# Optimization experiments

Measured on AMD Instinct MI355X. Metric: run time of the kernel, lower is better.

The kernel has to match this reference:

```python
import jax, jax.numpy as jnp
import numpy as np

B, W, K = 8, 128, 2048          # batch, window_size, n_features(=n_nodes)
D = 2 * W                        # embed_dim after the *2 in __init__ (embed_dim=None -> window_size)

def setup_inputs() -> dict:
    key = jax.random.key(0)
    k1, k2, k3, k4 = jax.random.split(key, 4)
    x = jax.random.normal(k1, (B, W, K), dtype=jnp.float32)
    # nn.Linear(2W -> D), stored as [in, out] so y = cat @ W_lin + b_lin
    lim = 1.0 / np.sqrt(2 * W)
    W_lin = jax.random.uniform(k2, (2 * W, D), dtype=jnp.float32, minval=-lim, maxval=lim)
    b_lin = jax.random.uniform(k3, (D,), dtype=jnp.float32, minval=-lim, maxval=lim)
    # a: xavier_uniform with gain=1.414 on shape (D, 1)
    a_lim = 1.414 * np.sqrt(6.0 / (D + 1))
    a = jax.random.uniform(k4, (D, 1), dtype=jnp.float32, minval=-a_lim, maxval=a_lim)
    bias = jnp.zeros((K, K), dtype=jnp.float32)
    return {"x": x, "W_lin": W_lin, "b_lin": b_lin, "a": a, "bias": bias}

def reference(x, W_lin, b_lin, a, bias):
    # x: [B, W, K] -> v: [B, K, W]
    v = jnp.transpose(x, (0, 2, 1))
    av = a[:, 0]                                  # [D]
    # lin(cat(v_i, v_j)) @ a == (v_i @ W1) @ a + (v_j @ W2) @ a + b_lin @ a
    # This avoids the O(K^2 * 2W) pairwise tensor; math identical to the original.
    W1, W2 = W_lin[:W], W_lin[W:]                 # each [W, D]
    u1 = jnp.einsum('bkw,wd,d->bk', v, W1, av)    # [B, K] source-side score
    u2 = jnp.einsum('bkw,wd,d->bk', v, W2, av)    # [B, K] target-side score
    e = u1[:, :, None] + u2[:, None, :] + jnp.dot(b_lin, av) + bias  # [B, K, K]
    attention = jax.nn.softmax(e, axis=2)         # dropout p=0.0 (eval) -> identity
    h = jax.nn.sigmoid(jnp.matmul(attention, v))  # [B, K, W]
    return jnp.transpose(h, (0, 2, 1))            # [B, W, K]
```

## Files before the change

kernel.cpp:

```cpp
#include <hip/hip_runtime.h>
#include <hip/hip_bf16.h>

#define B_ 8
#define W_ 128
#define K_ 2048
#define D_ 256
#define WX 144
#define NC 256

typedef __attribute__((ext_vector_type(8))) short bf16x8;
typedef __attribute__((ext_vector_type(4))) float f32x4;
typedef unsigned int u32;

static __device__ __forceinline__ short f2bf(float f) {
    unsigned int u = __float_as_uint(f);
    unsigned int r = (u + 0x7FFFu + ((u >> 16) & 1u)) >> 16;
    return (short)r;
}

__global__ void k_w2v(const float* __restrict__ W_lin, const float* __restrict__ a,
                      float* __restrict__ w2v) {
    int w = blockIdx.x, l = threadIdx.x;
    float4 rv = ((const float4*)(W_lin + (size_t)(W_ + w) * D_))[l];
    float4 av = ((const float4*)a)[l];
    float acc = rv.x * av.x + rv.y * av.y + rv.z * av.z + rv.w * av.w;
    for (int m = 1; m < 64; m <<= 1) acc += __shfl_xor(acc, m);
    if (l == 0) w2v[w] = acc;
}

__global__ __launch_bounds__(512) void k_pe(const float* __restrict__ x,
        const float* __restrict__ w2v, const float* __restrict__ bias,
        short* __restrict__ xbt, short* __restrict__ e2t) {
    __shared__ float sc[696];
    int tid = threadIdx.x;
    int wid = tid >> 6;
    int lane = tid & 63;

    if (blockIdx.x < 512) {
        if (tid < W_) sc[tid] = w2v[tid];
        __syncthreads();
        int q = tid & 31, cw = tid >> 5;
        int bk0 = blockIdx.x * 32;
        int b = bk0 >> 11;
        int k = (bk0 & (K_ - 1)) + q;
        const float* xp = x + ((size_t)b * W_ + cw * 8) * K_ + k;
        float xv[8];
        float acc = 0.f;
#pragma unroll
        for (int w = 0; w < 8; ++w) {
            xv[w] = xp[(size_t)w * K_];
            acc += xv[w] * sc[cw * 8 + w];
        }
        sc[128 + cw * 33 + q] = acc;
        __syncthreads();
        if (tid < 32) {
            float s = 0.f;
#pragma unroll
            for (int cc = 0; cc < 16; ++cc) s += sc[128 + cc * 33 + tid];
            sc[656 + tid] = __expf(s);
        }
        __syncthreads();
        float e1q = sc[656 + q];
        short* xo = xbt + (((size_t)b * NC + (k >> 3)) * WX + cw * 8) * 8 + (k & 7);
#pragma unroll
        for (int w = 0; w < 8; ++w) xo[w * 8] = f2bf(xv[w] * e1q);
        if (tid < 32) {
            int kk = (bk0 & (K_ - 1)) + tid;
            xbt[(((size_t)b * NC + (kk >> 3)) * WX + 128) * 8 + (kk & 7)] = f2bf(sc[656 + tid]);
        }
        if (tid >= 64 && tid < 124) {
            int id = tid - 64;
            int cl = id / 15, wz = 129 + id % 15;
            int c = ((bk0 & (K_ - 1)) >> 3) + cl;
            bf16x8 z = {0, 0, 0, 0, 0, 0, 0, 0};
            *(bf16x8*)(xbt + (((size_t)b * NC + c) * WX + wz) * 8) = z;
        }
    } else {
        int i0e = (int)(blockIdx.x - 512) * 4;
        {
            int r = tid >> 7, t128 = tid & 127;
            const float4* bp = (const float4*)(bias + (size_t)(i0e + r) * K_);
            float m = -1e30f;
#pragma unroll
            for (int s = 0; s < 4; ++s) {
                float4 v = bp[t128 + s * 128];
                m = fmaxf(m, fmaxf(fmaxf(v.x, v.y), fmaxf(v.z, v.w)));
            }
#pragma unroll
            for (int mm = 1; mm < 64; mm <<= 1) m = fmaxf(m, __shfl_xor(m, mm));
            if (lane == 0) sc[wid] = m;
        }
        __syncthreads();
        {
            int il = tid & 3, cg_ = tid >> 2;
            float mb = fmaxf(sc[il * 2], sc[il * 2 + 1]);
            int i = i0e + il;
            const float4* brow = (const float4*)(bias + (size_t)i * K_);
#pragma unroll
            for (int it = 0; it < 2; ++it) {
                int c = cg_ * 2 + it;
                float4 v0 = brow[c * 2];
                float4 v1 = brow[c * 2 + 1];
                bf16x8 o;
                o[0] = f2bf(__expf(v0.x - mb)); o[1] = f2bf(__expf(v0.y - mb));
                o[2] = f2bf(__expf(v0.z - mb)); o[3] = f2bf(__expf(v0.w - mb));
                o[4] = f2bf(__expf(v1.x - mb)); o[5] = f2bf(__expf(v1.y - mb));
                o[6] = f2bf(__expf(v1.z - mb)); o[7] = f2bf(__expf(v1.w - mb));
                *(bf16x8*)(e2t + ((size_t)c * K_ + i) * 8) = o;
            }
        }
    }
}

#define MF(a_, b_, c_) __builtin_amdgcn_mfma_f32_16x16x32_bf16(a_, b_, c_, 0, 0, 0)

#define GLLDS(gsrc, ldst) __builtin_amdgcn_global_load_lds(                      \
    (const u32 __attribute__((address_space(1)))*)(const void*)(gsrc),           \
    (u32 __attribute__((address_space(3)))*)(void*)(ldst), 16, 0, 0)

__global__ __launch_bounds__(1024, 4) void k_gemm(const short* __restrict__ e2t,
        const short* __restrict__ xbt, float* __restrict__ out) {
    __shared__ __align__(16) char Bb[73728];
    int blk  = blockIdx.x;
    int b    = blk & 7;
    int i0   = (blk >> 3) * 64;
    int tid  = threadIdx.x;
    int wid  = tid >> 6;
    int lane = tid & 63;
    int il   = lane & 15;
    int kg   = lane >> 4;
    int m    = wid & 3;
    int jq   = wid >> 2;

    int i0r = i0 + m * 16;
    const short* eA = e2t + (((size_t)(jq * 64 + kg)) * K_ + i0r + il) * 8;
    size_t xbase = ((size_t)b * NC + jq * 64 + kg) * WX + il;
    char* jbuf = Bb + jq * 18432;

#define STAGE(s_, bo_) do {                                                      \
    const short* _g = xbt + (xbase + (size_t)(s_) * 4 * WX) * 8;                 \
    char* _d = jbuf + (bo_);                                                     \
    for (int f = m; f < 9; f += 4)                                               \
        GLLDS(_g + f * 128, _d + f * 1024);                                      \
} while (0)

#define FA(dst_, s_) dst_ = *(const bf16x8*)(eA + (size_t)(s_) * 4 * K_ * 8)

    f32x4 q0{0,0,0,0}, q1{0,0,0,0}, q2{0,0,0,0}, q3{0,0,0,0}, q4{0,0,0,0},
          q5{0,0,0,0}, q6{0,0,0,0}, q7{0,0,0,0}, q8{0,0,0,0};

#define CONSUME(bo_, A_) do {                                                    \
    const char* _bp = jbuf + (bo_);                                              \
    bf16x8 b0 = *(const bf16x8*)(_bp +    0 + lane * 16);                        \
    bf16x8 b1 = *(const bf16x8*)(_bp + 1024 + lane * 16);                        \
    bf16x8 b2 = *(const bf16x8*)(_bp + 2048 + lane * 16);                        \
    bf16x8 b3 = *(const bf16x8*)(_bp + 3072 + lane * 16);                        \
    bf16x8 b4 = *(const bf16x8*)(_bp + 4096 + lane * 16);                        \
    bf16x8 b5 = *(const bf16x8*)(_bp + 5120 + lane * 16);                        \
    bf16x8 b6 = *(const bf16x8*)(_bp + 6144 + lane * 16);                        \
    bf16x8 b7 = *(const bf16x8*)(_bp + 7168 + lane * 16);                        \
    bf16x8 b8 = *(const bf16x8*)(_bp + 8192 + lane * 16);                        \
    __builtin_amdgcn_s_setprio(1);                                               \
    q0 = MF(A_, b0, q0); q1 = MF(A_, b1, q1); q2 = MF(A_, b2, q2);               \
    q3 = MF(A_, b3, q3); q4 = MF(A_, b4, q4); q5 = MF(A_, b5, q5);               \
    q6 = MF(A_, b6, q6); q7 = MF(A_, b7, q7); q8 = MF(A_, b8, q8);               \
    __builtin_amdgcn_s_setprio(0);                                               \
} while (0)

    bf16x8 AX, AY;
    STAGE(0, 0);
    FA(AX, 0);
    __syncthreads();
    for (int s = 0; s < 16; s += 2) {
        STAGE(s + 1, 9216);
        FA(AY, s + 1);
        CONSUME(0, AX);
        __syncthreads();
        if (s + 2 < 16) { STAGE(s + 2, 0); FA(AX, s + 2); }
        CONSUME(9216, AY);
        __syncthreads();
    }

    f32x4* R = (f32x4*)Bb;
#define DUMPQ(base_) do {                                                        \
    f32x4* _r = R + ((base_) + m * 9) * 64 + lane;                               \
    _r[0*64] = q0; _r[1*64] = q1; _r[2*64] = q2; _r[3*64] = q3; _r[4*64] = q4;   \
    _r[5*64] = q5; _r[6*64] = q6; _r[7*64] = q7; _r[8*64] = q8; } while (0)
#define GATHQ(base_) do {                                                        \
    f32x4* _r = R + ((base_) + m * 9) * 64 + lane;                               \
    q0 += _r[0*64]; q1 += _r[1*64]; q2 += _r[2*64]; q3 += _r[3*64];              \
    q4 += _r[4*64]; q5 += _r[5*64]; q6 += _r[6*64]; q7 += _r[7*64];              \
    q8 += _r[8*64]; } while (0)

    if (jq >= 2) DUMPQ((jq - 2) * 36);
    __syncthreads();
    if (jq < 2) GATHQ(jq * 36);
    __syncthreads();
    if (jq == 1) DUMPQ(0);
    __syncthreads();
    if (jq == 0) {
        GATHQ(0);
        float linv0 = 1.f / __shfl(q8[0], kg * 16);
        float linv1 = 1.f / __shfl(q8[1], kg * 16);
        float linv2 = 1.f / __shfl(q8[2], kg * 16);
        float linv3 = 1.f / __shfl(q8[3], kg * 16);
        float* ob = out + (size_t)b * W_ * K_ + i0r + kg * 4;
#define STQ(n_, q_) do {                                                         \
        float4 o;                                                                \
        o.x = 1.f / (1.f + __expf(-q_[0] * linv0));                              \
        o.y = 1.f / (1.f + __expf(-q_[1] * linv1));                              \
        o.z = 1.f / (1.f + __expf(-q_[2] * linv2));                              \
        o.w = 1.f / (1.f + __expf(-q_[3] * linv3));                              \
        *(float4*)(ob + (size_t)((n_) * 16 + il) * K_) = o; } while (0)
        STQ(0, q0); STQ(1, q1); STQ(2, q2); STQ(3, q3);
        STQ(4, q4); STQ(5, q5); STQ(6, q6); STQ(7, q7);
#undef STQ
    }
}

extern "C" void kernel_launch(void* const* d_in, const int* in_sizes, int n_in,
                              void* d_out, int out_size, void* d_ws, size_t ws_size,
                              hipStream_t stream) {
    const float* x     = (const float*)d_in[0];
    const float* W_lin = (const float*)d_in[1];
    const float* a     = (const float*)d_in[3];
    const float* bias  = (const float*)d_in[4];
    float* out = (float*)d_out;

    float* w2v = (float*)d_ws;
    short* xbt = (short*)(w2v + 128);
    short* e2t = xbt + (size_t)B_ * NC * WX * 8;

    k_w2v <<<128, 64, 0, stream>>>(W_lin, a, w2v);
    k_pe  <<<1024, 512, 0, stream>>>(x, w2v, bias, xbt, e2t);
    k_gemm<<<256, 1024, 0, stream>>>(e2t, xbt, out);
}
```

Before: 39.80 us.

## Deepen GEMM pipeline to four LDS stages with vmcnt-based waits

Replaces the two-buffer ping-pong main loop with a four-slot LDS ring buffer and a fully unrolled schedule that keeps two stages of global-to-LDS loads and A-fragment loads in flight. Each step waits on a per-wave vmcnt count and issues a bare s_barrier instead of a full __syncthreads, so memory latency is hidden further ahead of the MFMA work. In exchange LDS use doubles to 144 KB per block, which lowers occupancy. The hand-counted waitcnt values must match the number of outstanding loads for each wave role.

```diff
diff --git a/kernel.cpp b/kernel.cpp
--- a/kernel.cpp
+++ b/kernel.cpp
@@ -118,9 +118,12 @@
     (const u32 __attribute__((address_space(1)))*)(const void*)(gsrc),           \
     (u32 __attribute__((address_space(3)))*)(void*)(ldst), 16, 0, 0)
 
+#define WAITV(n_) asm volatile("s_waitcnt vmcnt(" #n_ ")" ::: "memory")
+#define BARR __builtin_amdgcn_s_barrier()
+
 __global__ __launch_bounds__(1024, 4) void k_gemm(const short* __restrict__ e2t,
         const short* __restrict__ xbt, float* __restrict__ out) {
-    __shared__ __align__(16) char Bb[73728];
+    __shared__ __align__(16) char Bb[147456];
     int blk  = blockIdx.x;
     int b    = blk & 7;
     int i0   = (blk >> 3) * 64;
@@ -135,22 +138,22 @@
     int i0r = i0 + m * 16;
     const short* eA = e2t + (((size_t)(jq * 64 + kg)) * K_ + i0r + il) * 8;
     size_t xbase = ((size_t)b * NC + jq * 64 + kg) * WX + il;
-    char* jbuf = Bb + jq * 18432;
-
-#define STAGE(s_, bo_) do {                                                      \
+    char* jbuf = Bb + jq * 36864;
+
+#define STG(s_) do {                                                             \
     const short* _g = xbt + (xbase + (size_t)(s_) * 4 * WX) * 8;                 \
-    char* _d = jbuf + (bo_);                                                     \
+    char* _d = jbuf + ((s_) & 3) * 9216;                                         \
     for (int f = m; f < 9; f += 4)                                               \
         GLLDS(_g + f * 128, _d + f * 1024);                                      \
 } while (0)
 
-#define FA(dst_, s_) dst_ = *(const bf16x8*)(eA + (size_t)(s_) * 4 * K_ * 8)
+#define FAix(sl_, s_) Ar##sl_ = *(const bf16x8*)(eA + (size_t)(s_) * 4 * K_ * 8)
 
     f32x4 q0{0,0,0,0}, q1{0,0,0,0}, q2{0,0,0,0}, q3{0,0,0,0}, q4{0,0,0,0},
           q5{0,0,0,0}, q6{0,0,0,0}, q7{0,0,0,0}, q8{0,0,0,0};
 
-#define CONSUME(bo_, A_) do {                                                    \
-    const char* _bp = jbuf + (bo_);                                              \
+#define CONS(s_, sl_) do {                                                       \
+    const char* _bp = jbuf + ((s_) & 3) * 9216;                                  \
     bf16x8 b0 = *(const bf16x8*)(_bp +    0 + lane * 16);                        \
     bf16x8 b1 = *(const bf16x8*)(_bp + 1024 + lane * 16);                        \
     bf16x8 b2 = *(const bf16x8*)(_bp + 2048 + lane * 16);                        \
@@ -161,25 +164,38 @@
     bf16x8 b7 = *(const bf16x8*)(_bp + 7168 + lane * 16);                        \
     bf16x8 b8 = *(const bf16x8*)(_bp + 8192 + lane * 16);                        \
     __builtin_amdgcn_s_setprio(1);                                               \
-    q0 = MF(A_, b0, q0); q1 = MF(A_, b1, q1); q2 = MF(A_, b2, q2);               \
-    q3 = MF(A_, b3, q3); q4 = MF(A_, b4, q4); q5 = MF(A_, b5, q5);               \
-    q6 = MF(A_, b6, q6); q7 = MF(A_, b7, q7); q8 = MF(A_, b8, q8);               \
+    q0 = MF(Ar##sl_, b0, q0); q1 = MF(Ar##sl_, b1, q1); q2 = MF(Ar##sl_, b2, q2);\
+    q3 = MF(Ar##sl_, b3, q3); q4 = MF(Ar##sl_, b4, q4); q5 = MF(Ar##sl_, b5, q5);\
+    q6 = MF(Ar##sl_, b6, q6); q7 = MF(Ar##sl_, b7, q7); q8 = MF(Ar##sl_, b8, q8);\
     __builtin_amdgcn_s_setprio(0);                                               \
 } while (0)
 
-    bf16x8 AX, AY;
-    STAGE(0, 0);
-    FA(AX, 0);
-    __syncthreads();
-    for (int s = 0; s < 16; s += 2) {
-        STAGE(s + 1, 9216);
-        FA(AY, s + 1);
-        CONSUME(0, AX);
-        __syncthreads();
-        if (s + 2 < 16) { STAGE(s + 2, 0); FA(AX, s + 2); }
-        CONSUME(9216, AY);
-        __syncthreads();
-    }
+#define STEP(s_, sl_, s2_, sl2_) do {                                            \
+    FAix(sl2_, s2_); STG(s2_);                                                   \
+    if (m == 0) WAITV(8); else WAITV(6);                                         \
+    BARR;                                                                        \
+    CONS(s_, sl_);                                                               \
+} while (0)
+
+    bf16x8 Ar0, Ar1, Ar2, Ar3;
+    FAix(0, 0); STG(0);
+    FAix(1, 1); STG(1);
+
+    STEP(0, 0, 2, 2);   STEP(1, 1, 3, 3);
+    STEP(2, 2, 4, 0);   STEP(3, 3, 5, 1);
+    STEP(4, 0, 6, 2);   STEP(5, 1, 7, 3);
+    STEP(6, 2, 8, 0);   STEP(7, 3, 9, 1);
+    STEP(8, 0, 10, 2);  STEP(9, 1, 11, 3);
+    STEP(10, 2, 12, 0); STEP(11, 3, 13, 1);
+    STEP(12, 0, 14, 2); STEP(13, 1, 15, 3);
+    if (m == 0) WAITV(4); else WAITV(3);
+    BARR;
+    CONS(14, 2);
+    WAITV(0);
+    BARR;
+    CONS(15, 3);
+
+    __syncthreads();
 
     f32x4* R = (f32x4*)Bb;
 #define DUMPQ(base_) do {                                                        \
```

New measurement: 35.51 us. 10.8% less time.
